# Optimization experiments

Measured on AMD Instinct MI355X. Metric: run time of the kernel, lower is better.

The kernel has to match this reference:

```python
import jax, jax.numpy as jnp
import numpy as np

IN_SIZE = 1024
CLASSES = 7
N = 50000
LN_EPS = 1e-5


def _chain(x, w, b, g, beta):
    # Linear -> (Dropout=identity at eval) -> LayerNorm -> GELU(exact erf)
    h = x @ w.T + b
    mu = jnp.mean(h, axis=-1, keepdims=True)
    var = jnp.var(h, axis=-1, keepdims=True)
    h = (h - mu) / jnp.sqrt(var + LN_EPS) * g + beta
    return jax.nn.gelu(h, approximate=False)


def setup_inputs() -> dict:
    key = jax.random.key(0)
    ks = jax.random.split(key, 16)
    d = IN_SIZE
    std = 1.0 / np.sqrt(d)
    inp = {
        "features": jax.random.normal(ks[0], (N, d), jnp.float32),
        "c": jax.random.normal(ks[1], (N, CLASSES), jnp.float32),
        "key_w": jax.random.uniform(ks[2], (d, d), jnp.float32, -std, std),
        "key_b": jax.random.uniform(ks[3], (d,), jnp.float32, -std, std),
        "key_g": jnp.ones((d,), jnp.float32),
        "key_beta": jnp.zeros((d,), jnp.float32),
        "query_w": jax.random.uniform(ks[4], (d, d), jnp.float32, -std, std),
        "query_b": jax.random.uniform(ks[5], (d,), jnp.float32, -std, std),
        "query_g": jnp.ones((d,), jnp.float32),
        "query_beta": jnp.zeros((d,), jnp.float32),
        "value_w": jax.random.uniform(ks[6], (d, d), jnp.float32, -std, std),
        "value_b": jax.random.uniform(ks[7], (d,), jnp.float32, -std, std),
        "value_g": jnp.ones((d,), jnp.float32),
        "value_beta": jnp.zeros((d,), jnp.float32),
        "head_w": jax.random.uniform(ks[8], (CLASSES, CLASSES, d), jnp.float32, -1.0 / np.sqrt(CLASSES * d), 1.0 / np.sqrt(CLASSES * d)),
        "head_b": jax.random.uniform(ks[9], (CLASSES,), jnp.float32, -1.0 / np.sqrt(CLASSES * d), 1.0 / np.sqrt(CLASSES * d)),
    }
    return inp


def reference(features, c, key_w, key_b, key_g, key_beta,
              query_w, query_b, query_g, query_beta,
              value_w, value_b, value_g, value_beta,
              head_w, head_b):
    K = _chain(features, key_w, key_b, key_g, key_beta)          # [N, d]
    V = _chain(K, value_w, value_b, value_g, value_beta)         # [N, d]
    Q = _chain(K, query_w, query_b, query_g, query_beta)         # [N, d]
    # critical (top-scoring) instance per class
    top_idx = jnp.argmax(c, axis=0)                              # [classes]
    m_feats = K[top_idx]                                         # [classes, d]
    q_max = _chain(m_feats, query_w, query_b, query_g, query_beta)  # [classes, d]
    A = Q @ q_max.T                                              # [N, classes]
    A = jax.nn.softmax(A / jnp.sqrt(jnp.float32(Q.shape[1])), axis=0)
    B = A.T @ V                                                  # [classes, d]
    # Conv1d(classes, classes, kernel_size=d) on [1, classes, d] -> full contraction
    C = jnp.einsum('ik,oik->o', B, head_w) + head_b              # [classes]
    C = C.reshape(1, -1)
    return (C, A, B.reshape(1, CLASSES, -1))
```

## Files before the change

### kernel.cpp

```cpp
#include <hip/hip_runtime.h>


typedef unsigned short u16;
typedef __attribute__((ext_vector_type(8))) short          bf16x8;
typedef __attribute__((ext_vector_type(8))) unsigned short u16x8;
typedef __attribute__((ext_vector_type(4))) unsigned short u16x4;
typedef __attribute__((ext_vector_type(4))) float          f32x4;

#define DDIM  1024
#define NROWS 50000
#define MP    50048
#define NCLS  7
#define MPD4  12512

__device__ __forceinline__ u16 f2bf(float f) {
  unsigned u = __float_as_uint(f);
  u = (u + 0x7FFFu + ((u >> 16) & 1u)) >> 16;
  return (u16)u;
}
__device__ __forceinline__ float bf2f(u16 h) {
  return __uint_as_float(((unsigned)h) << 16);
}
__device__ __forceinline__ float gelu(float x) {
  return 0.5f * x * (1.0f + erff(x * 0.70710678118654752f));
}

__device__ __forceinline__ void load16_lds(const u16* g, u16* l) {
  __builtin_amdgcn_global_load_lds(
      (const __attribute__((address_space(1))) unsigned int*)(const void*)g,
      (__attribute__((address_space(3))) unsigned int*)(void*)l, 16, 0, 0);
}

__global__ __launch_bounds__(256) void k_convert(const float* __restrict__ src,
                                                 u16* __restrict__ dst,
                                                 int rows_total, int rows_valid) {
  const size_t total = (size_t)rows_total * DDIM / 8;
  const size_t stride = (size_t)gridDim.x * blockDim.x;
  for (size_t i = (size_t)blockIdx.x * blockDim.x + threadIdx.x; i < total; i += stride) {
    const size_t e = i * 8;
    const int row = (int)(e >> 10);
    u16x8 o = {0, 0, 0, 0, 0, 0, 0, 0};
    if (row < rows_valid) {
      const float4* p = (const float4*)(src + e);
      float4 f0 = p[0], f1 = p[1];
      o[0] = f2bf(f0.x); o[1] = f2bf(f0.y); o[2] = f2bf(f0.z); o[3] = f2bf(f0.w);
      o[4] = f2bf(f1.x); o[5] = f2bf(f1.y); o[6] = f2bf(f1.z); o[7] = f2bf(f1.w);
    }
    *(u16x8*)(dst + e) = o;
  }
}

__global__ __launch_bounds__(256) void k_convw(const float* __restrict__ kw,
                                               const float* __restrict__ vw,
                                               const float* __restrict__ qw,
                                               u16* __restrict__ Wk,
                                               u16* __restrict__ Wvq) {
  const int w = blockIdx.x >> 7;
  const int b = blockIdx.x & 127;
  const float* src = (w == 0) ? kw : (w == 1) ? vw : qw;
  u16* dst = (w == 0) ? Wk : (Wvq + (size_t)(w - 1) * DDIM * DDIM);
  for (int i = b * 256 + threadIdx.x; i < DDIM * DDIM / 8; i += 128 * 256) {
    const float4* p = (const float4*)(src + (size_t)i * 8);
    float4 f0 = p[0], f1 = p[1];
    u16x8 o;
    o[0] = f2bf(f0.x); o[1] = f2bf(f0.y); o[2] = f2bf(f0.z); o[3] = f2bf(f0.w);
    o[4] = f2bf(f1.x); o[5] = f2bf(f1.y); o[6] = f2bf(f1.z); o[7] = f2bf(f1.w);
    *(u16x8*)(dst + (size_t)i * 8) = o;
  }
}

__global__ __launch_bounds__(256) void k_gemm_bt(const u16* __restrict__ A,
                                                 const u16* __restrict__ B,
                                                 u16* __restrict__ C,
                                                 int lnn, int ldc) {
  __shared__ __align__(16) u16 As[128 * 32];
  __shared__ __align__(16) u16 Bs[128 * 32];
  const int tid  = threadIdx.x;
  const int lane = tid & 63;
  const int cpx = gridDim.x >> 3;
  const int v   = (blockIdx.x & 7) * cpx + (blockIdx.x >> 3);
  const int m0 = (v >> lnn) * 128;
  const int n0 = (v & ((1 << lnn) - 1)) * 128;
  const int wid = tid >> 6;
  const int wr = (wid >> 1) * 64;
  const int wc = (wid & 1) * 64;

  const int rA = tid >> 2;
  const int cA = (tid & 3) * 8;
  const u16* Ap0 = A + (size_t)(m0 + rA) * DDIM + cA;
  const u16* Ap1 = Ap0 + (size_t)64 * DDIM;
  const u16* Bp0 = B + (size_t)(n0 + rA) * DDIM + cA;
  const u16* Bp1 = Bp0 + (size_t)64 * DDIM;
  const int wbase = wid * 64;
  u16* AsD0 = &As[(wbase)       * 8];
  u16* AsD1 = &As[(wbase + 256) * 8];
  u16* BsD0 = &Bs[(wbase)       * 8];
  u16* BsD1 = &Bs[(wbase + 256) * 8];

  f32x4 acc[4][4] = {};
  const int fr = lane & 15;
  const int kh = (lane >> 4) * 8;

  for (int k0 = 0; k0 < DDIM; k0 += 32) {
    __syncthreads();
    load16_lds(Ap0 + k0, AsD0);
    load16_lds(Ap1 + k0, AsD1);
    load16_lds(Bp0 + k0, BsD0);
    load16_lds(Bp1 + k0, BsD1);
    __syncthreads();
    bf16x8 a[4], b[4];
#pragma unroll
    for (int i = 0; i < 4; ++i) a[i] = *(const bf16x8*)&As[(wr + i * 16 + fr) * 32 + kh];
#pragma unroll
    for (int j = 0; j < 4; ++j) b[j] = *(const bf16x8*)&Bs[(wc + j * 16 + fr) * 32 + kh];
#pragma unroll
    for (int i = 0; i < 4; ++i)
#pragma unroll
      for (int j = 0; j < 4; ++j)
        acc[i][j] = __builtin_amdgcn_mfma_f32_16x16x32_bf16(a[i], b[j], acc[i][j], 0, 0, 0);
  }

  const int orow = (lane >> 4) * 4;
  const int ocol = lane & 15;
#pragma unroll
  for (int i = 0; i < 4; ++i)
#pragma unroll
    for (int j = 0; j < 4; ++j) {
      const size_t base = (size_t)(m0 + wr + i * 16 + orow) * ldc + (n0 + wc + j * 16 + ocol);
#pragma unroll
      for (int r = 0; r < 4; ++r)
        C[base + (size_t)r * ldc] = f2bf(acc[i][j][r]);
    }
}

__global__ __launch_bounds__(256) void k_ln_k(const u16* __restrict__ h,
                                              const float* __restrict__ bias,
                                              const float* __restrict__ g,
                                              const float* __restrict__ beta,
                                              u16* __restrict__ out) {
  const int lane = threadIdx.x & 63;
  const int row = blockIdx.x * 4 + (threadIdx.x >> 6);
  const int c0 = lane * 8;
  u16x8* op0 = (u16x8*)(out + (size_t)row * DDIM + c0);
  u16x8* op1 = (u16x8*)(out + (size_t)row * DDIM + 512 + c0);
  if (row >= NROWS) {
    u16x8 z = {0, 0, 0, 0, 0, 0, 0, 0};
    *op0 = z; *op1 = z;
    return;
  }
  u16x8 h0 = *(const u16x8*)(h + (size_t)row * DDIM + c0);
  u16x8 h1 = *(const u16x8*)(h + (size_t)row * DDIM + 512 + c0);
  float4 a0 = *(const float4*)(bias + c0), a1 = *(const float4*)(bias + c0 + 4);
  float4 a2 = *(const float4*)(bias + 512 + c0), a3 = *(const float4*)(bias + 512 + c0 + 4);
  const float ba[8] = {a0.x, a0.y, a0.z, a0.w, a1.x, a1.y, a1.z, a1.w};
  const float bb[8] = {a2.x, a2.y, a2.z, a2.w, a3.x, a3.y, a3.z, a3.w};
  float v0[8], v1[8];
  float s1 = 0.f, s2 = 0.f;
#pragma unroll
  for (int e = 0; e < 8; ++e) {
    v0[e] = bf2f(h0[e]) + ba[e];
    v1[e] = bf2f(h1[e]) + bb[e];
    s1 += v0[e] + v1[e];
    s2 += v0[e] * v0[e] + v1[e] * v1[e];
  }
#pragma unroll
  for (int m = 1; m < 64; m <<= 1) {
    s1 += __shfl_xor(s1, m, 64);
    s2 += __shfl_xor(s2, m, 64);
  }
  const float mu = s1 * (1.0f / 1024.0f);
  const float var = s2 * (1.0f / 1024.0f) - mu * mu;
  const float rs = rsqrtf(var + 1e-5f);
  float4 g0 = *(const float4*)(g + c0), g1 = *(const float4*)(g + c0 + 4);
  float4 g2 = *(const float4*)(g + 512 + c0), g3 = *(const float4*)(g + 512 + c0 + 4);
  float4 t0 = *(const float4*)(beta + c0), t1 = *(const float4*)(beta + c0 + 4);
  float4 t2 = *(const float4*)(beta + 512 + c0), t3 = *(const float4*)(beta + 512 + c0 + 4);
  const float ga[8] = {g0.x, g0.y, g0.z, g0.w, g1.x, g1.y, g1.z, g1.w};
  const float gb[8] = {g2.x, g2.y, g2.z, g2.w, g3.x, g3.y, g3.z, g3.w};
  const float ta[8] = {t0.x, t0.y, t0.z, t0.w, t1.x, t1.y, t1.z, t1.w};
  const float tb[8] = {t2.x, t2.y, t2.z, t2.w, t3.x, t3.y, t3.z, t3.w};
  u16x8 o0, o1;
#pragma unroll
  for (int e = 0; e < 8; ++e) {
    o0[e] = f2bf(gelu((v0[e] - mu) * rs * ga[e] + ta[e]));
    o1[e] = f2bf(gelu((v1[e] - mu) * rs * gb[e] + tb[e]));
  }
  *op0 = o0; *op1 = o1;
}

__global__ __launch_bounds__(256) void k_qmax(const u16* __restrict__ K,
                                              const int* __restrict__ top,
                                              const u16* __restrict__ Wq,
                                              const float* __restrict__ qb,
                                              const float* __restrict__ qg,
                                              const float* __restrict__ qbeta,
                                              u16* __restrict__ qm) {
  __shared__ __align__(16) u16 krow[DDIM];
  __shared__ float w1[4], w2[4];
  const int t = threadIdx.x;
  const int j = blockIdx.x;
  const u16* src = K + (size_t)top[j] * DDIM;
  if (t < 128) *(u16x8*)&krow[t * 8] = *(const u16x8*)&src[t * 8];
  __syncthreads();
  float acc[4];
#pragma unroll
  for (int c = 0; c < 4; ++c) {
    const int col = t * 4 + c;
    const u16x8* wp = (const u16x8*)(Wq + (size_t)col * DDIM);
    float s = 0.f;
    for (int kc = 0; kc < 128; ++kc) {
      u16x8 wv = wp[kc];
      u16x8 kv = *(const u16x8*)&krow[kc * 8];
#pragma unroll
      for (int e = 0; e < 8; ++e) s += bf2f(kv[e]) * bf2f(wv[e]);
    }
    acc[c] = s + qb[col];
  }
  float s1 = acc[0] + acc[1] + acc[2] + acc[3];
  float s2 = acc[0] * acc[0] + acc[1] * acc[1] + acc[2] * acc[2] + acc[3] * acc[3];
#pragma unroll
  for (int m = 1; m < 64; m <<= 1) {
    s1 += __shfl_xor(s1, m, 64);
    s2 += __shfl_xor(s2, m, 64);
  }
  if ((t & 63) == 0) { w1[t >> 6] = s1; w2[t >> 6] = s2; }
  __syncthreads();
  s1 = w1[0] + w1[1] + w1[2] + w1[3];
  s2 = w2[0] + w2[1] + w2[2] + w2[3];
  const float mu = s1 * (1.0f / 1024.0f);
  const float var = s2 * (1.0f / 1024.0f) - mu * mu;
  const float rs = rsqrtf(var + 1e-5f);
#pragma unroll
  for (int c = 0; c < 4; ++c) {
    const int col = t * 4 + c;
    qm[(size_t)j * DDIM + col] = f2bf(gelu((acc[c] - mu) * rs * qg[col] + qbeta[col]));
  }
}

__global__ __launch_bounds__(256) void k_ln_vq(const u16* __restrict__ h,
                                               const float* __restrict__ v_b,
                                               const float* __restrict__ v_g,
                                               const float* __restrict__ v_beta,
                                               const float* __restrict__ q_b,
                                               const float* __restrict__ q_g,
                                               const float* __restrict__ q_beta,
                                               const u16* __restrict__ qm,
                                               u16* __restrict__ V,
                                               float* __restrict__ logits) {
  __shared__ __align__(16) u16 sqm[NCLS * DDIM];
  const int tid = threadIdx.x;
  const int lane = tid & 63;
  const int half = (blockIdx.x >= MPD4) ? 1 : 0;
  const int rb = half ? (blockIdx.x - MPD4) : blockIdx.x;
  const int row = rb * 4 + (tid >> 6);
  if (half) {
    for (int i = tid; i < NCLS * DDIM / 8; i += 256)
      *(u16x8*)&sqm[i * 8] = *(const u16x8*)&qm[i * 8];
    __syncthreads();
  }
  if (row >= NROWS) return;
  const float* bias = half ? q_b : v_b;
  const float* gain = half ? q_g : v_g;
  const float* bet  = half ? q_beta : v_beta;
  const int c0 = lane * 8;
  const u16* hp = h + (size_t)row * 2048 + (size_t)half * DDIM;
  u16x8 h0 = *(const u16x8*)(hp + c0);
  u16x8 h1 = *(const u16x8*)(hp + 512 + c0);
  float4 a0 = *(const float4*)(bias + c0), a1 = *(const float4*)(bias + c0 + 4);
  float4 a2 = *(const float4*)(bias + 512 + c0), a3 = *(const float4*)(bias + 512 + c0 + 4);
  const float ba[8] = {a0.x, a0.y, a0.z, a0.w, a1.x, a1.y, a1.z, a1.w};
  const float bb[8] = {a2.x, a2.y, a2.z, a2.w, a3.x, a3.y, a3.z, a3.w};
  float v0[8], v1[8];
  float s1 = 0.f, s2 = 0.f;
#pragma unroll
  for (int e = 0; e < 8; ++e) {
    v0[e] = bf2f(h0[e]) + ba[e];
    v1[e] = bf2f(h1[e]) + bb[e];
    s1 += v0[e] + v1[e];
    s2 += v0[e] * v0[e] + v1[e] * v1[e];
  }
#pragma unroll
  for (int m = 1; m < 64; m <<= 1) {
    s1 += __shfl_xor(s1, m, 64);
    s2 += __shfl_xor(s2, m, 64);
  }
  const float mu = s1 * (1.0f / 1024.0f);
  const float var = s2 * (1.0f / 1024.0f) - mu * mu;
  const float rs = rsqrtf(var + 1e-5f);
  float4 g0 = *(const float4*)(gain + c0), g1 = *(const float4*)(gain + c0 + 4);
  float4 g2 = *(const float4*)(gain + 512 + c0), g3 = *(const float4*)(gain + 512 + c0 + 4);
  float4 t0 = *(const float4*)(bet + c0), t1 = *(const float4*)(bet + c0 + 4);
  float4 t2 = *(const float4*)(bet + 512 + c0), t3 = *(const float4*)(bet + 512 + c0 + 4);
  const float ga[8] = {g0.x, g0.y, g0.z, g0.w, g1.x, g1.y, g1.z, g1.w};
  const float gb[8] = {g2.x, g2.y, g2.z, g2.w, g3.x, g3.y, g3.z, g3.w};
  const float ta[8] = {t0.x, t0.y, t0.z, t0.w, t1.x, t1.y, t1.z, t1.w};
  const float tb[8] = {t2.x, t2.y, t2.z, t2.w, t3.x, t3.y, t3.z, t3.w};
  float y0[8], y1[8];
#pragma unroll
  for (int e = 0; e < 8; ++e) {
    y0[e] = gelu((v0[e] - mu) * rs * ga[e] + ta[e]);
    y1[e] = gelu((v1[e] - mu) * rs * gb[e] + tb[e]);
  }
  if (half == 0) {
    u16x8 o0, o1;
#pragma unroll
    for (int e = 0; e < 8; ++e) { o0[e] = f2bf(y0[e]); o1[e] = f2bf(y1[e]); }
    *(u16x8*)(V + (size_t)row * DDIM + c0) = o0;
    *(u16x8*)(V + (size_t)row * DDIM + 512 + c0) = o1;
  } else {
#pragma unroll
    for (int j = 0; j < NCLS; ++j) {
      u16x8 m0 = *(const u16x8*)&sqm[j * DDIM + c0];
      u16x8 m1 = *(const u16x8*)&sqm[j * DDIM + 512 + c0];
      float p = 0.f;
#pragma unroll
      for (int e = 0; e < 8; ++e) p += y0[e] * bf2f(m0[e]) + y1[e] * bf2f(m1[e]);
#pragma unroll
      for (int m = 1; m < 64; m <<= 1) p += __shfl_xor(p, m, 64);
      if (lane == 0) logits[(size_t)row * NCLS + j] = p * 0.03125f;
    }
  }
}

__global__ __launch_bounds__(256) void k_arg1(const float* __restrict__ c,
                                              float* __restrict__ pv,
                                              int* __restrict__ pi) {
  __shared__ float sv[256 * NCLS];
  __shared__ int   si[256 * NCLS];
  const int t = threadIdx.x;
  float bv[NCLS]; int bi[NCLS];
#pragma unroll
  for (int j = 0; j < NCLS; ++j) { bv[j] = -3.4e38f; bi[j] = 0x7fffffff; }
  for (int n = blockIdx.x * 256 + t; n < NROWS; n += 128 * 256) {
#pragma unroll
    for (int j = 0; j < NCLS; ++j) {
      const float v = c[(size_t)n * NCLS + j];
      if (v > bv[j]) { bv[j] = v; bi[j] = n; }
    }
  }
#pragma unroll
  for (int j = 0; j < NCLS; ++j) { sv[t * NCLS + j] = bv[j]; si[t * NCLS + j] = bi[j]; }
  __syncthreads();
  for (int s = 128; s > 0; s >>= 1) {
    if (t < s) {
#pragma unroll
      for (int j = 0; j < NCLS; ++j) {
        const float v2 = sv[(t + s) * NCLS + j]; const int i2 = si[(t + s) * NCLS + j];
        const float v1 = sv[t * NCLS + j];       const int i1 = si[t * NCLS + j];
        if (v2 > v1 || (v2 == v1 && i2 < i1)) { sv[t * NCLS + j] = v2; si[t * NCLS + j] = i2; }
      }
    }
    __syncthreads();
  }
  if (t < NCLS) { pv[blockIdx.x * NCLS + t] = sv[t]; pi[blockIdx.x * NCLS + t] = si[t]; }
}

__global__ void k_arg2(const float* __restrict__ pv, const int* __restrict__ pi,
                       int* __restrict__ top) {
  __shared__ float sv[128 * NCLS];
  __shared__ int   si[128 * NCLS];
  const int t = threadIdx.x;
#pragma unroll
  for (int j = 0; j < NCLS; ++j) { sv[t * NCLS + j] = pv[t * NCLS + j]; si[t * NCLS + j] = pi[t * NCLS + j]; }
  __syncthreads();
  for (int s = 64; s > 0; s >>= 1) {
    if (t < s) {
#pragma unroll
      for (int j = 0; j < NCLS; ++j) {
        const float v2 = sv[(t + s) * NCLS + j]; const int i2 = si[(t + s) * NCLS + j];
        const float v1 = sv[t * NCLS + j];       const int i1 = si[t * NCLS + j];
        if (v2 > v1 || (v2 == v1 && i2 < i1)) { sv[t * NCLS + j] = v2; si[t * NCLS + j] = i2; }
      }
    }
    __syncthreads();
  }
  if (t < NCLS) top[t] = si[t];
}

__global__ __launch_bounds__(256) void k_cmax_part(const float* __restrict__ logits,
                                                   float* __restrict__ pout) {
  __shared__ float sm[256 * NCLS];
  const int tid = threadIdx.x;
  float m[NCLS];
#pragma unroll
  for (int j = 0; j < NCLS; ++j) m[j] = -3.4e38f;
  const size_t stride = (size_t)gridDim.x * 256;
  for (size_t n = (size_t)blockIdx.x * 256 + tid; n < NROWS; n += stride)
#pragma unroll
    for (int j = 0; j < NCLS; ++j) m[j] = fmaxf(m[j], logits[n * NCLS + j]);
#pragma unroll
  for (int j = 0; j < NCLS; ++j) sm[tid * NCLS + j] = m[j];
  __syncthreads();
  for (int s = 128; s > 0; s >>= 1) {
    if (tid < s)
#pragma unroll
      for (int j = 0; j < NCLS; ++j)
        sm[tid * NCLS + j] = fmaxf(sm[tid * NCLS + j], sm[(tid + s) * NCLS + j]);
    __syncthreads();
  }
  if (tid < NCLS) pout[blockIdx.x * NCLS + tid] = sm[tid];
}

__global__ void k_cmax_fin(const float* __restrict__ pin, float* __restrict__ M, int nparts) {
  const int tid = threadIdx.x;
  if (tid < NCLS) {
    float m = -3.4e38f;
    for (int b = 0; b < nparts; ++b) m = fmaxf(m, pin[b * NCLS + tid]);
    M[tid] = m;
  }
}

__global__ __launch_bounds__(256) void k_csum_part(const float* __restrict__ logits,
                                                   const float* __restrict__ M,
                                                   float* __restrict__ pout) {
  __shared__ float sm[256 * NCLS];
  __shared__ float sM[NCLS];
  const int tid = threadIdx.x;
  if (tid < NCLS) sM[tid] = M[tid];
  __syncthreads();
  float s[NCLS];
#pragma unroll
  for (int j = 0; j < NCLS; ++j) s[j] = 0.f;
  const size_t stride = (size_t)gridDim.x * 256;
  for (size_t n = (size_t)blockIdx.x * 256 + tid; n < NROWS; n += stride)
#pragma unroll
    for (int j = 0; j < NCLS; ++j) s[j] += expf(logits[n * NCLS + j] - sM[j]);
#pragma unroll
  for (int j = 0; j < NCLS; ++j) sm[tid * NCLS + j] = s[j];
  __syncthreads();
  for (int st = 128; st > 0; st >>= 1) {
    if (tid < st)
#pragma unroll
      for (int j = 0; j < NCLS; ++j) sm[tid * NCLS + j] += sm[(tid + st) * NCLS + j];
    __syncthreads();
  }
  if (tid < NCLS) pout[blockIdx.x * NCLS + tid] = sm[tid];
}

__global__ void k_csum_fin(const float* __restrict__ pin, float* __restrict__ S, int nparts) {
  const int tid = threadIdx.x;
  if (tid < NCLS) {
    float s = 0.f;
    for (int b = 0; b < nparts; ++b) s += pin[b * NCLS + tid];
    S[tid] = s;
  }
}

__global__ __launch_bounds__(256) void k_bpart(const float* __restrict__ logits,
                                               const float* __restrict__ M,
                                               const float* __restrict__ S,
                                               const u16* __restrict__ V,
                                               float* __restrict__ Aout,
                                               float* __restrict__ Pb) {
  __shared__ float sA[98 * NCLS];
  __shared__ float sM[NCLS], sR[NCLS];
  const int t = threadIdx.x;
  if (t < NCLS) { sM[t] = M[t]; sR[t] = 1.0f / S[t]; }
  __syncthreads();
  const int n0 = blockIdx.x * 98;
  int cnt = NROWS - n0;
  cnt = cnt < 0 ? 0 : (cnt > 98 ? 98 : cnt);
  for (int idx = t; idx < cnt * NCLS; idx += 256) {
    const int j = idx % NCLS;
    const float a = expf(logits[(size_t)n0 * NCLS + idx] - sM[j]) * sR[j];
    sA[idx] = a;
    Aout[(size_t)n0 * NCLS + idx] = a;
  }
  __syncthreads();
  float acc[NCLS][4] = {};
  for (int r = 0; r < cnt; ++r) {
    u16x4 vv = *(const u16x4*)&V[(size_t)(n0 + r) * DDIM + t * 4];
    const float f0 = bf2f(vv[0]), f1 = bf2f(vv[1]), f2 = bf2f(vv[2]), f3 = bf2f(vv[3]);
#pragma unroll
    for (int j = 0; j < NCLS; ++j) {
      const float a = sA[r * NCLS + j];
      acc[j][0] += a * f0; acc[j][1] += a * f1; acc[j][2] += a * f2; acc[j][3] += a * f3;
    }
  }
#pragma unroll
  for (int j = 0; j < NCLS; ++j) {
    f32x4 o = {acc[j][0], acc[j][1], acc[j][2], acc[j][3]};
    *(f32x4*)&Pb[((size_t)blockIdx.x * NCLS + j) * DDIM + t * 4] = o;
  }
}

__global__ void k_bred(const float* __restrict__ Pb, float* __restrict__ Bout) {
  const int idx = blockIdx.x * 256 + threadIdx.x;
  if (idx >= NCLS * DDIM) return;
  float s = 0.f;
  for (int p = 0; p < 512; ++p) s += Pb[(size_t)p * NCLS * DDIM + idx];
  Bout[idx] = s;
}

__global__ __launch_bounds__(256) void k_head(const float* __restrict__ Bmat,
                                              const float* __restrict__ hw,
                                              const float* __restrict__ hb,
                                              float* __restrict__ Cout) {
  const int o = blockIdx.x, t = threadIdx.x;
  float p = 0.f;
  for (int idx = t; idx < NCLS * DDIM; idx += 256)
    p += Bmat[idx] * hw[(size_t)o * NCLS * DDIM + idx];
#pragma unroll
  for (int m = 1; m < 64; m <<= 1) p += __shfl_xor(p, m, 64);
  __shared__ float w[4];
  if ((t & 63) == 0) w[t >> 6] = p;
  __syncthreads();
  if (t == 0) Cout[o] = w[0] + w[1] + w[2] + w[3] + hb[o];
}

extern "C" void kernel_launch(void* const* d_in, const int* in_sizes, int n_in,
                              void* d_out, int out_size, void* d_ws, size_t ws_size,
                              hipStream_t stream) {
  const float* features   = (const float*)d_in[0];
  const float* c_in       = (const float*)d_in[1];
  const float* key_w      = (const float*)d_in[2];
  const float* key_b      = (const float*)d_in[3];
  const float* key_g      = (const float*)d_in[4];
  const float* key_beta   = (const float*)d_in[5];
  const float* query_w    = (const float*)d_in[6];
  const float* query_b    = (const float*)d_in[7];
  const float* query_g    = (const float*)d_in[8];
  const float* query_beta = (const float*)d_in[9];
  const float* value_w    = (const float*)d_in[10];
  const float* value_b    = (const float*)d_in[11];
  const float* value_g    = (const float*)d_in[12];
  const float* value_beta = (const float*)d_in[13];
  const float* head_w     = (const float*)d_in[14];
  const float* head_b     = (const float*)d_in[15];

  char* ws = (char*)d_ws;
  const size_t SZB = (size_t)MP * DDIM * 2;
  u16* Xb   = (u16*)ws;
  u16* HbVQ = Xb;
  u16* HbK  = (u16*)(ws + SZB);
  u16* Kb   = (u16*)(ws + 2 * SZB);
  u16* Vb   = Kb;
  size_t off = 3 * SZB;
  u16* Wk  = (u16*)(ws + off); off += (size_t)DDIM * DDIM * 2;
  u16* Wvq = (u16*)(ws + off); off += (size_t)2 * DDIM * DDIM * 2;
  float* logits = (float*)(ws + off); off += ((size_t)NROWS * NCLS * 4 + 255) & ~(size_t)255;
  float* Pb  = (float*)(ws + off); off += (size_t)512 * NCLS * DDIM * 4;
  u16* qm    = (u16*)(ws + off); off += ((size_t)NCLS * DDIM * 2 + 255) & ~(size_t)255;
  float* Pmax = (float*)(ws + off); off += ((size_t)128 * NCLS * 4 + 255) & ~(size_t)255;
  float* Psum = (float*)(ws + off); off += ((size_t)128 * NCLS * 4 + 255) & ~(size_t)255;
  float* argv = (float*)(ws + off); off += ((size_t)128 * NCLS * 4 + 255) & ~(size_t)255;
  int*   argi = (int*)  (ws + off); off += ((size_t)128 * NCLS * 4 + 255) & ~(size_t)255;
  float* Mmax = (float*)(ws + off); off += 256;
  float* Ssum = (float*)(ws + off); off += 256;
  int*   top  = (int*)  (ws + off); off += 256;

  float* Cout = (float*)d_out;
  float* Aout = Cout + NCLS;
  float* Bout = Aout + (size_t)NROWS * NCLS;

  k_arg1<<<128, 256, 0, stream>>>(c_in, argv, argi);
  k_arg2<<<1, 128, 0, stream>>>(argv, argi, top);
  k_convert<<<2048, 256, 0, stream>>>(features, Xb, MP, NROWS);
  k_convw<<<384, 256, 0, stream>>>(key_w, value_w, query_w, Wk, Wvq);

  k_gemm_bt<<<3128, 256, 0, stream>>>(Xb, Wk, HbK, 3, 1024);
  k_ln_k<<<MPD4, 256, 0, stream>>>(HbK, key_b, key_g, key_beta, Kb);

  k_qmax<<<NCLS, 256, 0, stream>>>(Kb, top, Wvq + (size_t)DDIM * DDIM,
                                   query_b, query_g, query_beta, qm);

  k_gemm_bt<<<6256, 256, 0, stream>>>(Kb, Wvq, HbVQ, 4, 2048);
  k_ln_vq<<<2 * MPD4, 256, 0, stream>>>(HbVQ, value_b, value_g, value_beta,
                                        query_b, query_g, query_beta, qm, Vb, logits);

  k_cmax_part<<<128, 256, 0, stream>>>(logits, Pmax);
  k_cmax_fin<<<1, 32, 0, stream>>>(Pmax, Mmax, 128);
  k_csum_part<<<128, 256, 0, stream>>>(logits, Mmax, Psum);
  k_csum_fin<<<1, 32, 0, stream>>>(Psum, Ssum, 128);

  k_bpart<<<512, 256, 0, stream>>>(logits, Mmax, Ssum, Vb, Aout, Pb);
  k_bred<<<28, 256, 0, stream>>>(Pb, Bout);
  k_head<<<NCLS, 256, 0, stream>>>(Bout, head_w, head_b, Cout);
}
```

Measured before the change: 829.5 us.

## Fuse GEMM with LayerNorm+GELU epilogue using full-row tiles and double buffering

```diff
diff --git a/kernel.cpp b/kernel.cpp
--- a/kernel.cpp
+++ b/kernel.cpp
@@ -10,8 +10,8 @@
 #define DDIM  1024
 #define NROWS 50000
 #define MP    50048
+#define NBLK  782
 #define NCLS  7
-#define MPD4  12512
 
 __device__ __forceinline__ u16 f2bf(float f) {
   unsigned u = __float_as_uint(f);
@@ -29,25 +29,6 @@
   __builtin_amdgcn_global_load_lds(
       (const __attribute__((address_space(1))) unsigned int*)(const void*)g,
       (__attribute__((address_space(3))) unsigned int*)(void*)l, 16, 0, 0);
-}
-
-__global__ __launch_bounds__(256) void k_convert(const float* __restrict__ src,
-                                                 u16* __restrict__ dst,
-                                                 int rows_total, int rows_valid) {
-  const size_t total = (size_t)rows_total * DDIM / 8;
-  const size_t stride = (size_t)gridDim.x * blockDim.x;
-  for (size_t i = (size_t)blockIdx.x * blockDim.x + threadIdx.x; i < total; i += stride) {
-    const size_t e = i * 8;
-    const int row = (int)(e >> 10);
-    u16x8 o = {0, 0, 0, 0, 0, 0, 0, 0};
-    if (row < rows_valid) {
-      const float4* p = (const float4*)(src + e);
-      float4 f0 = p[0], f1 = p[1];
-      o[0] = f2bf(f0.x); o[1] = f2bf(f0.y); o[2] = f2bf(f0.z); o[3] = f2bf(f0.w);
-      o[4] = f2bf(f1.x); o[5] = f2bf(f1.y); o[6] = f2bf(f1.z); o[7] = f2bf(f1.w);
-    }
-    *(u16x8*)(dst + e) = o;
-  }
 }
 
 __global__ __launch_bounds__(256) void k_convw(const float* __restrict__ kw,
@@ -69,256 +50,206 @@
   }
 }
 
-__global__ __launch_bounds__(256) void k_gemm_bt(const u16* __restrict__ A,
-                                                 const u16* __restrict__ B,
-                                                 u16* __restrict__ C,
-                                                 int lnn, int ldc) {
-  __shared__ __align__(16) u16 As[128 * 32];
-  __shared__ __align__(16) u16 Bs[128 * 32];
-  const int tid  = threadIdx.x;
+template<int AFP32>
+__global__ __launch_bounds__(512, 2) void k_gemm_ln(const float* __restrict__ Af,
+                                                    const u16* __restrict__ Ab,
+                                                    const u16* __restrict__ Bw,
+                                                    const float* __restrict__ bias,
+                                                    const float* __restrict__ gain,
+                                                    const float* __restrict__ beta,
+                                                    u16* __restrict__ Out) {
+  const int tid = threadIdx.x;
+  const int v = (blockIdx.x & 7) * 98 + (blockIdx.x >> 3);
+  if (v >= NBLK) return;
+  const int r0 = v * 64;
   const int lane = tid & 63;
-  const int cpx = gridDim.x >> 3;
-  const int v   = (blockIdx.x & 7) * cpx + (blockIdx.x >> 3);
-  const int m0 = (v >> lnn) * 128;
-  const int n0 = (v & ((1 << lnn) - 1)) * 128;
   const int wid = tid >> 6;
-  const int wr = (wid >> 1) * 64;
-  const int wc = (wid & 1) * 64;
-
-  const int rA = tid >> 2;
-  const int cA = (tid & 3) * 8;
-  const u16* Ap0 = A + (size_t)(m0 + rA) * DDIM + cA;
-  const u16* Ap1 = Ap0 + (size_t)64 * DDIM;
-  const u16* Bp0 = B + (size_t)(n0 + rA) * DDIM + cA;
-  const u16* Bp1 = Bp0 + (size_t)64 * DDIM;
-  const int wbase = wid * 64;
-  u16* AsD0 = &As[(wbase)       * 8];
-  u16* AsD1 = &As[(wbase + 256) * 8];
-  u16* BsD0 = &Bs[(wbase)       * 8];
-  u16* BsD1 = &Bs[(wbase + 256) * 8];
-
-  f32x4 acc[4][4] = {};
   const int fr = lane & 15;
-  const int kh = (lane >> 4) * 8;
-
-  for (int k0 = 0; k0 < DDIM; k0 += 32) {
+  const int T = lane >> 4;
+  const int cb = wid * 128;
+  const int sw16 = (T ^ ((fr >> 1) & 3)) << 3;
+
+  __shared__ __align__(16) u16 As[2][64 * 32];
+  __shared__ __align__(16) u16 Bs[2][1024 * 32];
+  __shared__ float red1[8][64], red2[8][64];
+  __shared__ float muS[64], rsS[64];
+
+  f32x4 acc[4][8] = {};
+
+  const int arow = tid >> 2;
+  const int aslotl = tid & 3;
+  const int asw = aslotl ^ ((arow >> 1) & 3);
+
+#define STAGE_B(K0, BUF) do {                                                  \
+    _Pragma("unroll") for (int l = 0; l < 8; ++l) {                            \
+      const int c = l * 512 + tid;                                             \
+      const int row_ = c >> 2;                                                 \
+      const int slot_ = (c & 3) ^ ((row_ >> 1) & 3);                           \
+      load16_lds(Bw + (size_t)row_ * DDIM + (K0) + slot_ * 8,                  \
+                 &Bs[BUF][(size_t)c * 8]);                                     \
+    } } while (0)
+
+#define COMPUTE(BUF) do {                                                      \
+    const u16* _As = &As[BUF][0];                                              \
+    const u16* _Bs = &Bs[BUF][0];                                              \
+    bf16x8 af[4]; bf16x8 bfr[8];                                               \
+    _Pragma("unroll") for (int mi = 0; mi < 4; ++mi)                           \
+      af[mi] = *(const bf16x8*)&_As[(mi * 16 + fr) * 32 + sw16];               \
+    _Pragma("unroll") for (int nj = 0; nj < 8; ++nj)                           \
+      bfr[nj] = *(const bf16x8*)&_Bs[(cb + nj * 16 + fr) * 32 + sw16];         \
+    _Pragma("unroll") for (int mi = 0; mi < 4; ++mi)                           \
+      _Pragma("unroll") for (int nj = 0; nj < 8; ++nj)                         \
+        acc[mi][nj] = __builtin_amdgcn_mfma_f32_16x16x32_bf16(af[mi], bfr[nj], \
+                                                              acc[mi][nj], 0, 0, 0); \
+  } while (0)
+
+  STAGE_B(0, 0);
+  if (tid < 256) {
+    const int grow = r0 + arow;
+    if (AFP32) {
+      u16x8 o = {0, 0, 0, 0, 0, 0, 0, 0};
+      if (grow < NROWS) {
+        const float* sp = Af + (size_t)grow * DDIM + aslotl * 8;
+        float4 fa = *(const float4*)sp, fb = *(const float4*)(sp + 4);
+        o[0] = f2bf(fa.x); o[1] = f2bf(fa.y); o[2] = f2bf(fa.z); o[3] = f2bf(fa.w);
+        o[4] = f2bf(fb.x); o[5] = f2bf(fb.y); o[6] = f2bf(fb.z); o[7] = f2bf(fb.w);
+      }
+      *(u16x8*)&As[0][arow * 32 + (asw << 3)] = o;
+    } else {
+      load16_lds(Ab + (size_t)grow * DDIM + asw * 8, &As[0][tid * 8]);
+    }
+  }
+  __syncthreads();
+
+  for (int kt = 0; kt < 32; ++kt) {
+    const int cur = kt & 1;
+    float4 fa = {0.f, 0.f, 0.f, 0.f}, fb = {0.f, 0.f, 0.f, 0.f};
+    bool av = false;
+    if (kt < 31) {
+      const int k0 = (kt + 1) * 32;
+      if (AFP32) {
+        if (tid < 256) {
+          const int grow = r0 + arow;
+          av = grow < NROWS;
+          if (av) {
+            const float* sp = Af + (size_t)grow * DDIM + k0 + aslotl * 8;
+            fa = *(const float4*)sp; fb = *(const float4*)(sp + 4);
+          }
+        }
+      } else {
+        if (tid < 256)
+          load16_lds(Ab + (size_t)(r0 + arow) * DDIM + k0 + asw * 8,
+                     &As[cur ^ 1][tid * 8]);
+      }
+      STAGE_B(k0, cur ^ 1);
+    }
+    COMPUTE(cur);
+    if (AFP32) {
+      if (kt < 31 && tid < 256) {
+        u16x8 o = {0, 0, 0, 0, 0, 0, 0, 0};
+        if (av) {
+          o[0] = f2bf(fa.x); o[1] = f2bf(fa.y); o[2] = f2bf(fa.z); o[3] = f2bf(fa.w);
+          o[4] = f2bf(fb.x); o[5] = f2bf(fb.y); o[6] = f2bf(fb.z); o[7] = f2bf(fb.w);
+        }
+        *(u16x8*)&As[cur ^ 1][arow * 32 + (asw << 3)] = o;
+      }
+    }
     __syncthreads();
-    load16_lds(Ap0 + k0, AsD0);
-    load16_lds(Ap1 + k0, AsD1);
-    load16_lds(Bp0 + k0, BsD0);
-    load16_lds(Bp1 + k0, BsD1);
-    __syncthreads();
-    bf16x8 a[4], b[4];
-#pragma unroll
-    for (int i = 0; i < 4; ++i) a[i] = *(const bf16x8*)&As[(wr + i * 16 + fr) * 32 + kh];
-#pragma unroll
-    for (int j = 0; j < 4; ++j) b[j] = *(const bf16x8*)&Bs[(wc + j * 16 + fr) * 32 + kh];
-#pragma unroll
-    for (int i = 0; i < 4; ++i)
-#pragma unroll
-      for (int j = 0; j < 4; ++j)
-        acc[i][j] = __builtin_amdgcn_mfma_f32_16x16x32_bf16(a[i], b[j], acc[i][j], 0, 0, 0);
-  }
-
-  const int orow = (lane >> 4) * 4;
-  const int ocol = lane & 15;
-#pragma unroll
-  for (int i = 0; i < 4; ++i)
-#pragma unroll
-    for (int j = 0; j < 4; ++j) {
-      const size_t base = (size_t)(m0 + wr + i * 16 + orow) * ldc + (n0 + wc + j * 16 + ocol);
-#pragma unroll
-      for (int r = 0; r < 4; ++r)
-        C[base + (size_t)r * ldc] = f2bf(acc[i][j][r]);
-    }
-}
-
-__global__ __launch_bounds__(256) void k_ln_k(const u16* __restrict__ h,
-                                              const float* __restrict__ bias,
-                                              const float* __restrict__ g,
-                                              const float* __restrict__ beta,
-                                              u16* __restrict__ out) {
-  const int lane = threadIdx.x & 63;
-  const int row = blockIdx.x * 4 + (threadIdx.x >> 6);
-  const int c0 = lane * 8;
-  u16x8* op0 = (u16x8*)(out + (size_t)row * DDIM + c0);
-  u16x8* op1 = (u16x8*)(out + (size_t)row * DDIM + 512 + c0);
-  if (row >= NROWS) {
-    u16x8 z = {0, 0, 0, 0, 0, 0, 0, 0};
-    *op0 = z; *op1 = z;
-    return;
-  }
-  u16x8 h0 = *(const u16x8*)(h + (size_t)row * DDIM + c0);
-  u16x8 h1 = *(const u16x8*)(h + (size_t)row * DDIM + 512 + c0);
-  float4 a0 = *(const float4*)(bias + c0), a1 = *(const float4*)(bias + c0 + 4);
-  float4 a2 = *(const float4*)(bias + 512 + c0), a3 = *(const float4*)(bias + 512 + c0 + 4);
-  const float ba[8] = {a0.x, a0.y, a0.z, a0.w, a1.x, a1.y, a1.z, a1.w};
-  const float bb[8] = {a2.x, a2.y, a2.z, a2.w, a3.x, a3.y, a3.z, a3.w};
-  float v0[8], v1[8];
-  float s1 = 0.f, s2 = 0.f;
-#pragma unroll
-  for (int e = 0; e < 8; ++e) {
-    v0[e] = bf2f(h0[e]) + ba[e];
-    v1[e] = bf2f(h1[e]) + bb[e];
-    s1 += v0[e] + v1[e];
-    s2 += v0[e] * v0[e] + v1[e] * v1[e];
-  }
-#pragma unroll
-  for (int m = 1; m < 64; m <<= 1) {
-    s1 += __shfl_xor(s1, m, 64);
-    s2 += __shfl_xor(s2, m, 64);
-  }
-  const float mu = s1 * (1.0f / 1024.0f);
-  const float var = s2 * (1.0f / 1024.0f) - mu * mu;
-  const float rs = rsqrtf(var + 1e-5f);
-  float4 g0 = *(const float4*)(g + c0), g1 = *(const float4*)(g + c0 + 4);
-  float4 g2 = *(const float4*)(g + 512 + c0), g3 = *(const float4*)(g + 512 + c0 + 4);
-  float4 t0 = *(const float4*)(beta + c0), t1 = *(const float4*)(beta + c0 + 4);
-  float4 t2 = *(const float4*)(beta + 512 + c0), t3 = *(const float4*)(beta + 512 + c0 + 4);
-  const float ga[8] = {g0.x, g0.y, g0.z, g0.w, g1.x, g1.y, g1.z, g1.w};
-  const float gb[8] = {g2.x, g2.y, g2.z, g2.w, g3.x, g3.y, g3.z, g3.w};
-  const float ta[8] = {t0.x, t0.y, t0.z, t0.w, t1.x, t1.y, t1.z, t1.w};
-  const float tb[8] = {t2.x, t2.y, t2.z, t2.w, t3.x, t3.y, t3.z, t3.w};
-  u16x8 o0, o1;
-#pragma unroll
-  for (int e = 0; e < 8; ++e) {
-    o0[e] = f2bf(gelu((v0[e] - mu) * rs * ga[e] + ta[e]));
-    o1[e] = f2bf(gelu((v1[e] - mu) * rs * gb[e] + tb[e]));
-  }
-  *op0 = o0; *op1 = o1;
-}
-
-__global__ __launch_bounds__(256) void k_qmax(const u16* __restrict__ K,
-                                              const int* __restrict__ top,
-                                              const u16* __restrict__ Wq,
-                                              const float* __restrict__ qb,
-                                              const float* __restrict__ qg,
-                                              const float* __restrict__ qbeta,
-                                              u16* __restrict__ qm) {
-  __shared__ __align__(16) u16 krow[DDIM];
-  __shared__ float w1[4], w2[4];
-  const int t = threadIdx.x;
-  const int j = blockIdx.x;
-  const u16* src = K + (size_t)top[j] * DDIM;
-  if (t < 128) *(u16x8*)&krow[t * 8] = *(const u16x8*)&src[t * 8];
-  __syncthreads();
-  float acc[4];
-#pragma unroll
-  for (int c = 0; c < 4; ++c) {
-    const int col = t * 4 + c;
-    const u16x8* wp = (const u16x8*)(Wq + (size_t)col * DDIM);
-    float s = 0.f;
-    for (int kc = 0; kc < 128; ++kc) {
-      u16x8 wv = wp[kc];
-      u16x8 kv = *(const u16x8*)&krow[kc * 8];
-#pragma unroll
-      for (int e = 0; e < 8; ++e) s += bf2f(kv[e]) * bf2f(wv[e]);
-    }
-    acc[c] = s + qb[col];
-  }
-  float s1 = acc[0] + acc[1] + acc[2] + acc[3];
-  float s2 = acc[0] * acc[0] + acc[1] * acc[1] + acc[2] * acc[2] + acc[3] * acc[3];
-#pragma unroll
-  for (int m = 1; m < 64; m <<= 1) {
-    s1 += __shfl_xor(s1, m, 64);
-    s2 += __shfl_xor(s2, m, 64);
-  }
-  if ((t & 63) == 0) { w1[t >> 6] = s1; w2[t >> 6] = s2; }
-  __syncthreads();
-  s1 = w1[0] + w1[1] + w1[2] + w1[3];
-  s2 = w2[0] + w2[1] + w2[2] + w2[3];
-  const float mu = s1 * (1.0f / 1024.0f);
-  const float var = s2 * (1.0f / 1024.0f) - mu * mu;
-  const float rs = rsqrtf(var + 1e-5f);
-#pragma unroll
-  for (int c = 0; c < 4; ++c) {
-    const int col = t * 4 + c;
-    qm[(size_t)j * DDIM + col] = f2bf(gelu((acc[c] - mu) * rs * qg[col] + qbeta[col]));
-  }
-}
-
-__global__ __launch_bounds__(256) void k_ln_vq(const u16* __restrict__ h,
-                                               const float* __restrict__ v_b,
-                                               const float* __restrict__ v_g,
-                                               const float* __restrict__ v_beta,
-                                               const float* __restrict__ q_b,
-                                               const float* __restrict__ q_g,
-                                               const float* __restrict__ q_beta,
-                                               const u16* __restrict__ qm,
-                                               u16* __restrict__ V,
-                                               float* __restrict__ logits) {
-  __shared__ __align__(16) u16 sqm[NCLS * DDIM];
+  }
+#undef STAGE_B
+#undef COMPUTE
+
+  float bsv[8], gsv[8], tsv[8];
+#pragma unroll
+  for (int nj = 0; nj < 8; ++nj) {
+    const int col = cb + nj * 16 + fr;
+    bsv[nj] = bias[col]; gsv[nj] = gain[col]; tsv[nj] = beta[col];
+  }
+  float s1a[4][4], s2a[4][4];
+#pragma unroll
+  for (int mi = 0; mi < 4; ++mi)
+#pragma unroll
+    for (int r = 0; r < 4; ++r) {
+      float s1 = 0.f, s2 = 0.f;
+#pragma unroll
+      for (int nj = 0; nj < 8; ++nj) {
+        const float h = acc[mi][nj][r] + bsv[nj];
+        s1 += h; s2 += h * h;
+      }
+#pragma unroll
+      for (int m = 1; m < 16; m <<= 1) {
+        s1 += __shfl_xor(s1, m, 64);
+        s2 += __shfl_xor(s2, m, 64);
+      }
+      s1a[mi][r] = s1; s2a[mi][r] = s2;
+    }
+  if (fr == 0) {
+#pragma unroll
+    for (int mi = 0; mi < 4; ++mi)
+#pragma unroll
+      for (int r = 0; r < 4; ++r) {
+        const int row = mi * 16 + T * 4 + r;
+        red1[wid][row] = s1a[mi][r];
+        red2[wid][row] = s2a[mi][r];
+      }
+  }
+  __syncthreads();
+  if (tid < 64) {
+    float S1 = 0.f, S2 = 0.f;
+#pragma unroll
+    for (int w = 0; w < 8; ++w) { S1 += red1[w][tid]; S2 += red2[w][tid]; }
+    const float mu = S1 * (1.0f / 1024.0f);
+    const float var = S2 * (1.0f / 1024.0f) - mu * mu;
+    muS[tid] = mu;
+    rsS[tid] = rsqrtf(var + 1e-5f);
+  }
+  __syncthreads();
+#pragma unroll
+  for (int mi = 0; mi < 4; ++mi)
+#pragma unroll
+    for (int r = 0; r < 4; ++r) {
+      const int row = mi * 16 + T * 4 + r;
+      const int grow = r0 + row;
+      const float mu = muS[row], rs = rsS[row];
+      const bool valid = grow < NROWS;
+#pragma unroll
+      for (int nj = 0; nj < 8; ++nj) {
+        const float h = acc[mi][nj][r] + bsv[nj];
+        const float y = gelu((h - mu) * rs * gsv[nj] + tsv[nj]);
+        Out[(size_t)grow * DDIM + cb + nj * 16 + fr] = valid ? f2bf(y) : (u16)0;
+      }
+    }
+}
+
+__global__ __launch_bounds__(256) void k_logits(const u16* __restrict__ Q,
+                                                const int* __restrict__ top,
+                                                float* __restrict__ logits) {
+  __shared__ __align__(16) u16 qm[NCLS * DDIM];
   const int tid = threadIdx.x;
+  for (int i = tid; i < NCLS * (DDIM / 8); i += 256) {
+    const int j = i >> 7;
+    const int ch = i & 127;
+    *(u16x8*)&qm[j * DDIM + ch * 8] = *(const u16x8*)&Q[(size_t)top[j] * DDIM + ch * 8];
+  }
+  __syncthreads();
   const int lane = tid & 63;
-  const int half = (blockIdx.x >= MPD4) ? 1 : 0;
-  const int rb = half ? (blockIdx.x - MPD4) : blockIdx.x;
-  const int row = rb * 4 + (tid >> 6);
-  if (half) {
-    for (int i = tid; i < NCLS * DDIM / 8; i += 256)
-      *(u16x8*)&sqm[i * 8] = *(const u16x8*)&qm[i * 8];
-    __syncthreads();
-  }
-  if (row >= NROWS) return;
-  const float* bias = half ? q_b : v_b;
-  const float* gain = half ? q_g : v_g;
-  const float* bet  = half ? q_beta : v_beta;
-  const int c0 = lane * 8;
-  const u16* hp = h + (size_t)row * 2048 + (size_t)half * DDIM;
-  u16x8 h0 = *(const u16x8*)(hp + c0);
-  u16x8 h1 = *(const u16x8*)(hp + 512 + c0);
-  float4 a0 = *(const float4*)(bias + c0), a1 = *(const float4*)(bias + c0 + 4);
-  float4 a2 = *(const float4*)(bias + 512 + c0), a3 = *(const float4*)(bias + 512 + c0 + 4);
-  const float ba[8] = {a0.x, a0.y, a0.z, a0.w, a1.x, a1.y, a1.z, a1.w};
-  const float bb[8] = {a2.x, a2.y, a2.z, a2.w, a3.x, a3.y, a3.z, a3.w};
-  float v0[8], v1[8];
-  float s1 = 0.f, s2 = 0.f;
-#pragma unroll
-  for (int e = 0; e < 8; ++e) {
-    v0[e] = bf2f(h0[e]) + ba[e];
-    v1[e] = bf2f(h1[e]) + bb[e];
-    s1 += v0[e] + v1[e];
-    s2 += v0[e] * v0[e] + v1[e] * v1[e];
-  }
-#pragma unroll
-  for (int m = 1; m < 64; m <<= 1) {
-    s1 += __shfl_xor(s1, m, 64);
-    s2 += __shfl_xor(s2, m, 64);
-  }
-  const float mu = s1 * (1.0f / 1024.0f);
-  const float var = s2 * (1.0f / 1024.0f) - mu * mu;
-  const float rs = rsqrtf(var + 1e-5f);
-  float4 g0 = *(const float4*)(gain + c0), g1 = *(const float4*)(gain + c0 + 4);
-  float4 g2 = *(const float4*)(gain + 512 + c0), g3 = *(const float4*)(gain + 512 + c0 + 4);
-  float4 t0 = *(const float4*)(bet + c0), t1 = *(const float4*)(bet + c0 + 4);
-  float4 t2 = *(const float4*)(bet + 512 + c0), t3 = *(const float4*)(bet + 512 + c0 + 4);
-  const float ga[8] = {g0.x, g0.y, g0.z, g0.w, g1.x, g1.y, g1.z, g1.w};
-  const float gb[8] = {g2.x, g2.y, g2.z, g2.w, g3.x, g3.y, g3.z, g3.w};
-  const float ta[8] = {t0.x, t0.y, t0.z, t0.w, t1.x, t1.y, t1.z, t1.w};
-  const float tb[8] = {t2.x, t2.y, t2.z, t2.w, t3.x, t3.y, t3.z, t3.w};
-  float y0[8], y1[8];
-#pragma unroll
-  for (int e = 0; e < 8; ++e) {
-    y0[e] = gelu((v0[e] - mu) * rs * ga[e] + ta[e]);
-    y1[e] = gelu((v1[e] - mu) * rs * gb[e] + tb[e]);
-  }
-  if (half == 0) {
-    u16x8 o0, o1;
-#pragma unroll
-    for (int e = 0; e < 8; ++e) { o0[e] = f2bf(y0[e]); o1[e] = f2bf(y1[e]); }
-    *(u16x8*)(V + (size_t)row * DDIM + c0) = o0;
-    *(u16x8*)(V + (size_t)row * DDIM + 512 + c0) = o1;
-  } else {
-#pragma unroll
-    for (int j = 0; j < NCLS; ++j) {
-      u16x8 m0 = *(const u16x8*)&sqm[j * DDIM + c0];
-      u16x8 m1 = *(const u16x8*)&sqm[j * DDIM + 512 + c0];
-      float p = 0.f;
-#pragma unroll
-      for (int e = 0; e < 8; ++e) p += y0[e] * bf2f(m0[e]) + y1[e] * bf2f(m1[e]);
-#pragma unroll
-      for (int m = 1; m < 64; m <<= 1) p += __shfl_xor(p, m, 64);
-      if (lane == 0) logits[(size_t)row * NCLS + j] = p * 0.03125f;
-    }
+  const int n = blockIdx.x * 4 + (tid >> 6);
+  if (n >= NROWS) return;
+  const u16x8* qp = (const u16x8*)(Q + (size_t)n * DDIM + lane * 16);
+  u16x8 q0 = qp[0], q1 = qp[1];
+  float qf[16];
+#pragma unroll
+  for (int e = 0; e < 8; ++e) { qf[e] = bf2f(q0[e]); qf[e + 8] = bf2f(q1[e]); }
+#pragma unroll
+  for (int j = 0; j < NCLS; ++j) {
+    const u16x8* mp = (const u16x8*)&qm[j * DDIM + lane * 16];
+    u16x8 m0 = mp[0], m1 = mp[1];
+    float p = 0.f;
+#pragma unroll
+    for (int e = 0; e < 8; ++e) p += qf[e] * bf2f(m0[e]) + qf[e + 8] * bf2f(m1[e]);
+#pragma unroll
+    for (int m = 1; m < 64; m <<= 1) p += __shfl_xor(p, m, 64);
+    if (lane == 0) logits[(size_t)n * NCLS + j] = p * 0.03125f;
   }
 }
 
@@ -401,22 +332,17 @@
   if (tid < NCLS) pout[blockIdx.x * NCLS + tid] = sm[tid];
 }
 
-__global__ void k_cmax_fin(const float* __restrict__ pin, float* __restrict__ M, int nparts) {
-  const int tid = threadIdx.x;
-  if (tid < NCLS) {
-    float m = -3.4e38f;
-    for (int b = 0; b < nparts; ++b) m = fmaxf(m, pin[b * NCLS + tid]);
-    M[tid] = m;
-  }
-}
-
 __global__ __launch_bounds__(256) void k_csum_part(const float* __restrict__ logits,
-                                                   const float* __restrict__ M,
+                                                   const float* __restrict__ Pmax,
                                                    float* __restrict__ pout) {
   __shared__ float sm[256 * NCLS];
   __shared__ float sM[NCLS];
   const int tid = threadIdx.x;
-  if (tid < NCLS) sM[tid] = M[tid];
+  if (tid < NCLS) {
+    float m = -3.4e38f;
+    for (int b = 0; b < 128; ++b) m = fmaxf(m, Pmax[b * NCLS + tid]);
+    sM[tid] = m;
+  }
   __syncthreads();
   float s[NCLS];
 #pragma unroll
@@ -437,25 +363,22 @@
   if (tid < NCLS) pout[blockIdx.x * NCLS + tid] = sm[tid];
 }
 
-__global__ void k_csum_fin(const float* __restrict__ pin, float* __restrict__ S, int nparts) {
-  const int tid = threadIdx.x;
-  if (tid < NCLS) {
-    float s = 0.f;
-    for (int b = 0; b < nparts; ++b) s += pin[b * NCLS + tid];
-    S[tid] = s;
-  }
-}
-
 __global__ __launch_bounds__(256) void k_bpart(const float* __restrict__ logits,
-                                               const float* __restrict__ M,
-                                               const float* __restrict__ S,
+                                               const float* __restrict__ Pmax,
+                                               const float* __restrict__ Psum,
                                                const u16* __restrict__ V,
                                                float* __restrict__ Aout,
                                                float* __restrict__ Pb) {
   __shared__ float sA[98 * NCLS];
   __shared__ float sM[NCLS], sR[NCLS];
   const int t = threadIdx.x;
-  if (t < NCLS) { sM[t] = M[t]; sR[t] = 1.0f / S[t]; }
+  if (t < NCLS) {
+    float m = -3.4e38f;
+    for (int b = 0; b < 128; ++b) m = fmaxf(m, Pmax[b * NCLS + t]);
+    float s = 0.f;
+    for (int b = 0; b < 128; ++b) s += Psum[b * NCLS + t];
+    sM[t] = m; sR[t] = 1.0f / s;
+  }
   __syncthreads();
   const int n0 = blockIdx.x * 98;
   int cnt = NROWS - n0;
@@ -530,23 +453,18 @@
 
   char* ws = (char*)d_ws;
   const size_t SZB = (size_t)MP * DDIM * 2;
-  u16* Xb   = (u16*)ws;
-  u16* HbVQ = Xb;
-  u16* HbK  = (u16*)(ws + SZB);
-  u16* Kb   = (u16*)(ws + 2 * SZB);
-  u16* Vb   = Kb;
+  u16* Kb = (u16*)ws;
+  u16* Vb = (u16*)(ws + SZB);
+  u16* Qb = (u16*)(ws + 2 * SZB);
   size_t off = 3 * SZB;
   u16* Wk  = (u16*)(ws + off); off += (size_t)DDIM * DDIM * 2;
   u16* Wvq = (u16*)(ws + off); off += (size_t)2 * DDIM * DDIM * 2;
   float* logits = (float*)(ws + off); off += ((size_t)NROWS * NCLS * 4 + 255) & ~(size_t)255;
   float* Pb  = (float*)(ws + off); off += (size_t)512 * NCLS * DDIM * 4;
-  u16* qm    = (u16*)(ws + off); off += ((size_t)NCLS * DDIM * 2 + 255) & ~(size_t)255;
   float* Pmax = (float*)(ws + off); off += ((size_t)128 * NCLS * 4 + 255) & ~(size_t)255;
   float* Psum = (float*)(ws + off); off += ((size_t)128 * NCLS * 4 + 255) & ~(size_t)255;
   float* argv = (float*)(ws + off); off += ((size_t)128 * NCLS * 4 + 255) & ~(size_t)255;
   int*   argi = (int*)  (ws + off); off += ((size_t)128 * NCLS * 4 + 255) & ~(size_t)255;
-  float* Mmax = (float*)(ws + off); off += 256;
-  float* Ssum = (float*)(ws + off); off += 256;
   int*   top  = (int*)  (ws + off); off += 256;
 
   float* Cout = (float*)d_out;
@@ -555,25 +473,20 @@
 
   k_arg1<<<128, 256, 0, stream>>>(c_in, argv, argi);
   k_arg2<<<1, 128, 0, stream>>>(argv, argi, top);
-  k_convert<<<2048, 256, 0, stream>>>(features, Xb, MP, NROWS);
   k_convw<<<384, 256, 0, stream>>>(key_w, value_w, query_w, Wk, Wvq);
 
-  k_gemm_bt<<<3128, 256, 0, stream>>>(Xb, Wk, HbK, 3, 1024);
-  k_ln_k<<<MPD4, 256, 0, stream>>>(HbK, key_b, key_g, key_beta, Kb);
-
-  k_qmax<<<NCLS, 256, 0, stream>>>(Kb, top, Wvq + (size_t)DDIM * DDIM,
-                                   query_b, query_g, query_beta, qm);
-
-  k_gemm_bt<<<6256, 256, 0, stream>>>(Kb, Wvq, HbVQ, 4, 2048);
-  k_ln_vq<<<2 * MPD4, 256, 0, stream>>>(HbVQ, value_b, value_g, value_beta,
-                                        query_b, query_g, query_beta, qm, Vb, logits);
-
+  k_gemm_ln<1><<<784, 512, 0, stream>>>(features, nullptr, Wk,
+                                        key_b, key_g, key_beta, Kb);
+  k_gemm_ln<0><<<784, 512, 0, stream>>>(nullptr, Kb, Wvq,
+                                        value_b, value_g, value_beta, Vb);
+  k_gemm_ln<0><<<784, 512, 0, stream>>>(nullptr, Kb, Wvq + (size_t)DDIM * DDIM,
+                                        query_b, query_g, query_beta, Qb);
+
+  k_logits<<<(NROWS + 3) / 4, 256, 0, stream>>>(Qb, top, logits);
   k_cmax_part<<<128, 256, 0, stream>>>(logits, Pmax);
-  k_cmax_fin<<<1, 32, 0, stream>>>(Pmax, Mmax, 128);
-  k_csum_part<<<128, 256, 0, stream>>>(logits, Mmax, Psum);
-  k_csum_fin<<<1, 32, 0, stream>>>(Psum, Ssum, 128);
-
-  k_bpart<<<512, 256, 0, stream>>>(logits, Mmax, Ssum, Vb, Aout, Pb);
+  k_csum_part<<<128, 256, 0, stream>>>(logits, Pmax, Psum);
+
+  k_bpart<<<512, 256, 0, stream>>>(logits, Pmax, Psum, Vb, Aout, Pb);
   k_bred<<<28, 256, 0, stream>>>(Pb, Bout);
   k_head<<<NCLS, 256, 0, stream>>>(Bout, head_w, head_b, Cout);
 }
```

Measured after the change: 1.132 ms. +36.4%, slower.
